# Kernel tuning notes

Hardware: AMD Instinct MI355X
Metric: run time of the kernel (lower is better)

Reference implementation:

```python
import jax, jax.numpy as jnp
import numpy as np

EMBED_DIM = 1024
N = 8192


def setup_inputs() -> dict:
    key = jax.random.key(0)
    k1, k2, k3 = jax.random.split(key, 3)
    inputs = jax.random.normal(k1, (N, EMBED_DIM), dtype=jnp.float32)
    rotation = jax.random.normal(k2, (EMBED_DIM, EMBED_DIM), dtype=jnp.float32)
    entangle = jax.random.normal(k3, (EMBED_DIM, EMBED_DIM), dtype=jnp.float32)
    return {"inputs": inputs, "rotation": rotation, "entangle": entangle}


def reference(inputs, rotation, entangle):
    # inputs: [N, D]; rotation/entangle: [D, D]
    query = inputs @ rotation          # [N, D]
    key = inputs @ entangle            # [N, D]
    scale = 1.0 / np.sqrt(inputs.shape[-1]).astype(np.float32)
    logits = (query @ key.T) * scale   # [N, N]
    scores = jax.nn.softmax(logits, axis=-1)
    return scores @ inputs             # [N, D]
```

## Files before the change

kernel.cpp:

```cpp
#include <hip/hip_runtime.h>


typedef _Float16 f16;
typedef _Float16 f16x4 __attribute__((ext_vector_type(4)));
typedef _Float16 f16x8 __attribute__((ext_vector_type(8)));
typedef float    f32x4 __attribute__((ext_vector_type(4)));
typedef unsigned int u32;

#define N_ROWS 8192
#define D_DIM  1024
#define LOG2E  1.44269504088896340736f

__device__ __forceinline__ void gload_lds16(const void* g, void* l) {
  __builtin_amdgcn_global_load_lds(
      (const __attribute__((address_space(1))) u32*)g,
      (__attribute__((address_space(3))) u32*)l, 16, 0, 0);
}

__device__ __forceinline__ f16x8 read_frag(const f16* tile, int row, int lane) {
  int kb = ((lane >> 4) & 3) << 4;
  int phys = row * 64 + (kb ^ (((row >> 1) & 3) << 4));
  return *(const f16x8*)((const char*)tile + phys);
}

__device__ __forceinline__ f16x8 read_frag64(const f16* tile, int row, int lane, int ks2) {
  int kb = ks2 * 64 + (((lane >> 4) & 3) << 4);
  int phys = row * 128 + (kb ^ ((row & 7) << 4));
  return *(const f16x8*)((const char*)tile + phys);
}

__global__ __launch_bounds__(256) void splitk(const float* __restrict__ in,
                                              f16* __restrict__ hi, f16* __restrict__ lo,
                                              int n4) {
  int i = blockIdx.x * 256 + threadIdx.x;
  if (i >= n4) return;
  float4 v = ((const float4*)in)[i];
  float vv[4] = {v.x, v.y, v.z, v.w};
  f16x4 h, l;
#pragma unroll
  for (int j = 0; j < 4; ++j) {
    f16 hh = (f16)vv[j];
    h[j] = hh;
    l[j] = (f16)(vv[j] - (float)hh);
  }
  *(f16x4*)(hi + (size_t)i * 4) = h;
  *(f16x4*)(lo + (size_t)i * 4) = l;
}

__global__ __launch_bounds__(256) void transpose_cast(const float* __restrict__ X,
                                                      f16* __restrict__ Xt) {
  __shared__ float tile[32][33];
  int bx = blockIdx.x, by = blockIdx.y;
  int tx = threadIdx.x & 31, ty0 = threadIdx.x >> 5;
#pragma unroll
  for (int r = 0; r < 4; ++r) {
    int ty = ty0 + r * 8;
    tile[ty][tx] = X[(size_t)(by * 32 + ty) * D_DIM + bx * 32 + tx];
  }
  __syncthreads();
#pragma unroll
  for (int r = 0; r < 4; ++r) {
    int ty = ty0 + r * 8;
    Xt[(size_t)(bx * 32 + ty) * N_ROWS + by * 32 + tx] = (f16)tile[tx][ty];
  }
}

__global__ __launch_bounds__(256) void gemm_abt_s(
    const f16* __restrict__ Ahi, const f16* __restrict__ Alo,
    const f16* __restrict__ Bhi, const f16* __restrict__ Blo,
    int Ncols, f16* __restrict__ Chi, f16* __restrict__ Clo) {
  __shared__ __align__(16) f16 lds[4 * 4096];
  const int t = threadIdx.x, w = t >> 6, l = t & 63;
  const int bn = blockIdx.x, bm = blockIdx.y;
  const int wr = (w >> 1) * 64, wc = (w & 1) * 64;
  const char* srcs[4];
  srcs[0] = (const char*)(Ahi + (size_t)bm * 128 * 1024);
  srcs[1] = (const char*)(Alo + (size_t)bm * 128 * 1024);
  srcs[2] = (const char*)(Bhi + (size_t)bn * 128 * 1024);
  srcs[3] = (const char*)(Blo + (size_t)bn * 128 * 1024);
  f32x4 acc[4][4] = {};
  for (int ks = 0; ks < 32; ++ks) {
#pragma unroll
    for (int tt = 0; tt < 4; ++tt)
#pragma unroll
      for (int j = 0; j < 2; ++j) {
        int seg = j * 4 + w;
        int p = seg * 1024 + l * 16;
        int r = p >> 6;
        int sw = (p & 63) ^ (((r >> 1) & 3) << 4);
        gload_lds16(srcs[tt] + (size_t)r * 2048 + ks * 64 + sw,
                    (char*)lds + tt * 8192 + seg * 1024);
      }
    __syncthreads();
    f16x8 ah[4], al[4], bh[4], bl[4];
#pragma unroll
    for (int m = 0; m < 4; ++m) {
      int row = wr + m * 16 + (l & 15);
      ah[m] = read_frag(lds, row, l);
      al[m] = read_frag(lds + 4096, row, l);
    }
#pragma unroll
    for (int n = 0; n < 4; ++n) {
      int row = wc + n * 16 + (l & 15);
      bh[n] = read_frag(lds + 8192, row, l);
      bl[n] = read_frag(lds + 12288, row, l);
    }
#pragma unroll
    for (int m = 0; m < 4; ++m)
#pragma unroll
      for (int n = 0; n < 4; ++n) {
        acc[m][n] = __builtin_amdgcn_mfma_f32_16x16x32_f16(ah[m], bh[n], acc[m][n], 0, 0, 0);
        acc[m][n] = __builtin_amdgcn_mfma_f32_16x16x32_f16(ah[m], bl[n], acc[m][n], 0, 0, 0);
        acc[m][n] = __builtin_amdgcn_mfma_f32_16x16x32_f16(al[m], bh[n], acc[m][n], 0, 0, 0);
      }
    __syncthreads();
  }
#pragma unroll
  for (int m = 0; m < 4; ++m)
#pragma unroll
    for (int n = 0; n < 4; ++n)
#pragma unroll
      for (int j = 0; j < 4; ++j) {
        int row = bm * 128 + wr + m * 16 + ((l >> 4) << 2) + j;
        int col = bn * 128 + wc + n * 16 + (l & 15);
        float v = acc[m][n][j];
        size_t idx = (size_t)row * Ncols + col;
        f16 hh = (f16)v;
        Chi[idx] = hh;
        Clo[idx] = (f16)(v - (float)hh);
      }
}

__global__ __launch_bounds__(512, 2) void gemm_abt_big(
    const f16* __restrict__ Ahi, const f16* __restrict__ Alo,
    const f16* __restrict__ Bhi, const f16* __restrict__ Blo,
    float scale, float* __restrict__ C) {
  __shared__ __align__(16) f16 lds[2][4 * 8192];
  const int t = threadIdx.x, w = t >> 6, l = t & 63;
  const int bn = blockIdx.x, bm = blockIdx.y;
  const int wm = w >> 2, wn = w & 3;
  const char* srcs[4];
  srcs[0] = (const char*)(Ahi + (size_t)bm * 256 * 1024);
  srcs[1] = (const char*)(Alo + (size_t)bm * 256 * 1024);
  srcs[2] = (const char*)(Bhi + (size_t)bn * 256 * 1024);
  srcs[3] = (const char*)(Blo + (size_t)bn * 256 * 1024);

#define STAGE_BIG(buf, kt)                                                   \
  {                                                                          \
    _Pragma("unroll") for (int rnd = 0; rnd < 8; ++rnd) {                    \
      int phys = rnd * 8192 + t * 16;           \
      int tile = phys >> 14;                                                 \
      int r = (phys & 16383) >> 6;                                           \
      int q = phys & 63;                                                     \
      int sw = q ^ (((r >> 1) & 3) << 4);                                    \
      gload_lds16(srcs[tile] + (size_t)r * 2048 + (kt) * 64 + sw,            \
                  (char*)&lds[buf][0] + phys);                               \
    }                                                                        \
  }

  f32x4 acc[8][4] = {};
  STAGE_BIG(0, 0);
  __syncthreads();
  int cur = 0;
  for (int kt = 0; kt < 32; ++kt) {
    if (kt < 31) STAGE_BIG(cur ^ 1, kt + 1);
    const f16* Lb = &lds[cur][0];
    f16x8 bh[4], bl[4];
#pragma unroll
    for (int n = 0; n < 4; ++n) {
      int row = wn * 64 + n * 16 + (l & 15);
      bh[n] = read_frag(Lb + 16384, row, l);
      bl[n] = read_frag(Lb + 24576, row, l);
    }
#pragma unroll
    for (int m = 0; m < 8; ++m) {
      int row = wm * 128 + m * 16 + (l & 15);
      f16x8 ah = read_frag(Lb, row, l);
      f16x8 al = read_frag(Lb + 8192, row, l);
#pragma unroll
      for (int n = 0; n < 4; ++n) {
        acc[m][n] = __builtin_amdgcn_mfma_f32_16x16x32_f16(ah, bh[n], acc[m][n], 0, 0, 0);
        acc[m][n] = __builtin_amdgcn_mfma_f32_16x16x32_f16(ah, bl[n], acc[m][n], 0, 0, 0);
        acc[m][n] = __builtin_amdgcn_mfma_f32_16x16x32_f16(al, bh[n], acc[m][n], 0, 0, 0);
      }
    }
    __syncthreads();
    cur ^= 1;
  }
#undef STAGE_BIG
#pragma unroll
  for (int m = 0; m < 8; ++m)
#pragma unroll
    for (int n = 0; n < 4; ++n)
#pragma unroll
      for (int j = 0; j < 4; ++j) {
        int row = bm * 256 + wm * 128 + m * 16 + ((l >> 4) << 2) + j;
        int col = bn * 256 + wn * 64 + n * 16 + (l & 15);
        C[(size_t)row * N_ROWS + col] = acc[m][n][j] * scale;
      }
}

__global__ __launch_bounds__(256) void pexp(const float* __restrict__ L,
                                            f16* __restrict__ P) {
  const int row = blockIdx.x, t = threadIdx.x, w = t >> 6, l = t & 63;
  const float4* p = (const float4*)(L + (size_t)row * N_ROWS);
  __shared__ float red[8];
  float4 v[8];
#pragma unroll
  for (int i = 0; i < 8; ++i) v[i] = p[t + i * 256];
  float mx = -3.4e38f;
#pragma unroll
  for (int i = 0; i < 8; ++i)
    mx = fmaxf(mx, fmaxf(fmaxf(v[i].x, v[i].y), fmaxf(v[i].z, v[i].w)));
#pragma unroll
  for (int off = 32; off; off >>= 1) mx = fmaxf(mx, __shfl_xor(mx, off));
  if (l == 0) red[w] = mx;
  __syncthreads();
  mx = fmaxf(fmaxf(red[0], red[1]), fmaxf(red[2], red[3]));
  float e[8][4];
  float s = 0.f;
#pragma unroll
  for (int i = 0; i < 8; ++i) {
    e[i][0] = exp2f((v[i].x - mx) * LOG2E);
    e[i][1] = exp2f((v[i].y - mx) * LOG2E);
    e[i][2] = exp2f((v[i].z - mx) * LOG2E);
    e[i][3] = exp2f((v[i].w - mx) * LOG2E);
    s += (e[i][0] + e[i][1]) + (e[i][2] + e[i][3]);
  }
#pragma unroll
  for (int off = 32; off; off >>= 1) s += __shfl_xor(s, off);
  if (l == 0) red[4 + w] = s;
  __syncthreads();
  float sinv = 1.0f / (red[4] + red[5] + red[6] + red[7]);
  f16* prow = P + (size_t)row * 16384;
#pragma unroll
  for (int i = 0; i < 8; ++i) {
    f16x4 h;
    h[0] = (f16)(e[i][0] * sinv);
    h[1] = (f16)(e[i][1] * sinv);
    h[2] = (f16)(e[i][2] * sinv);
    h[3] = (f16)(e[i][3] * sinv);
    *(f16x4*)(prow + (size_t)(t + i * 256) * 4) = h;
  }
}

__global__ __launch_bounds__(256) void gemm_pv(
    const f16* __restrict__ P,
    const f16* __restrict__ Xt,
    float* __restrict__ out) {
  __shared__ __align__(16) f16 ldsA[64 * 64];
  __shared__ __align__(16) f16 ldsB[128 * 64];
  const int t = threadIdx.x, w = t >> 6, l = t & 63;
  const int bn = blockIdx.x, bm = blockIdx.y;
  const int wr = (w >> 1) * 32, wc = (w & 1) * 64;
  const char* Abase = (const char*)(P + (size_t)bm * 64 * 16384);
  const char* Bbase = (const char*)(Xt + (size_t)bn * 128 * 8192);
  f32x4 acc[2][4] = {};
  for (int ks = 0; ks < 128; ++ks) {
#pragma unroll
    for (int s = 0; s < 2; ++s) {
      int p = s * 4096 + t * 16;
      int r = p >> 7, q = p & 127;
      int sq = q ^ ((r & 7) << 4);
      gload_lds16(Abase + (size_t)r * 32768 + ks * 128 + sq, (char*)ldsA + p);
    }
#pragma unroll
    for (int s = 0; s < 4; ++s) {
      int p = s * 4096 + t * 16;
      int r = p >> 7, q = p & 127;
      int sq = q ^ ((r & 7) << 4);
      gload_lds16(Bbase + (size_t)r * 16384 + ks * 128 + sq, (char*)ldsB + p);
    }
    __syncthreads();
#pragma unroll
    for (int ks2 = 0; ks2 < 2; ++ks2) {
      f16x8 a[2], b[4];
#pragma unroll
      for (int m = 0; m < 2; ++m) a[m] = read_frag64(ldsA, wr + m * 16 + (l & 15), l, ks2);
#pragma unroll
      for (int n = 0; n < 4; ++n) b[n] = read_frag64(ldsB, wc + n * 16 + (l & 15), l, ks2);
#pragma unroll
      for (int m = 0; m < 2; ++m)
#pragma unroll
        for (int n = 0; n < 4; ++n)
          acc[m][n] = __builtin_amdgcn_mfma_f32_16x16x32_f16(a[m], b[n], acc[m][n], 0, 0, 0);
    }
    __syncthreads();
  }
#pragma unroll
  for (int m = 0; m < 2; ++m)
#pragma unroll
    for (int n = 0; n < 4; ++n)
#pragma unroll
      for (int j = 0; j < 4; ++j) {
        int row = bm * 64 + wr + m * 16 + ((l >> 4) << 2) + j;
        int col = bn * 128 + wc + n * 16 + (l & 15);
        out[(size_t)row * D_DIM + col] = acc[m][n][j];
      }
}

extern "C" void kernel_launch(void* const* d_in, const int* in_sizes, int n_in,
                              void* d_out, int out_size, void* d_ws, size_t ws_size,
                              hipStream_t stream) {
  const float* X = (const float*)d_in[0];
  const float* R = (const float*)d_in[1];
  const float* E = (const float*)d_in[2];
  float* out = (float*)d_out;

  char* p = (char*)d_ws;
  auto alloc = [&](size_t bytes) -> char* {
    char* r = p;
    p += (bytes + 255) & ~(size_t)255;
    return r;
  };
  f16* Xhi = (f16*)alloc((size_t)N_ROWS * D_DIM * 2);
  f16* Xlo = (f16*)alloc((size_t)N_ROWS * D_DIM * 2);
  f16* Yhi = (f16*)alloc((size_t)N_ROWS * D_DIM * 2);
  f16* Ylo = (f16*)alloc((size_t)N_ROWS * D_DIM * 2);
  f16* Xt  = (f16*)alloc((size_t)N_ROWS * D_DIM * 2);
  float* Lbuf = (float*)p;
  size_t front = (size_t)(p - (char*)d_ws);

  char* tail = (char*)d_ws + ws_size;
  auto alloct = [&](size_t bytes) -> char* {
    tail = (char*)(((uintptr_t)tail - bytes) & ~(uintptr_t)255);
    return tail;
  };
  f16* Rhi  = (f16*)alloct((size_t)D_DIM * D_DIM * 2);
  f16* Rlo  = (f16*)alloct((size_t)D_DIM * D_DIM * 2);
  f16* Ehi  = (f16*)alloct((size_t)D_DIM * D_DIM * 2);
  f16* Elo  = (f16*)alloct((size_t)D_DIM * D_DIM * 2);
  f16* Mthi = (f16*)alloct((size_t)D_DIM * D_DIM * 2);
  f16* Mtlo = (f16*)alloct((size_t)D_DIM * D_DIM * 2);

  size_t avail = ws_size > front ? ws_size - front : 0;
  int CH = (int)(avail / ((size_t)N_ROWS * 4));
  if (CH > N_ROWS) CH = N_ROWS;
  CH &= ~255;
  if (CH < 256) CH = 256;

  splitk<<<dim3((N_ROWS * D_DIM / 4 + 255) / 256), 256, 0, stream>>>(X, Xhi, Xlo, N_ROWS * D_DIM / 4);
  splitk<<<dim3((D_DIM * D_DIM / 4 + 255) / 256), 256, 0, stream>>>(R, Rhi, Rlo, D_DIM * D_DIM / 4);
  splitk<<<dim3((D_DIM * D_DIM / 4 + 255) / 256), 256, 0, stream>>>(E, Ehi, Elo, D_DIM * D_DIM / 4);
  transpose_cast<<<dim3(D_DIM / 32, N_ROWS / 32), 256, 0, stream>>>(X, Xt);

  gemm_abt_s<<<dim3(8, 8), 256, 0, stream>>>(Ehi, Elo, Rhi, Rlo, D_DIM, Mthi, Mtlo);
  gemm_abt_s<<<dim3(8, 64), 256, 0, stream>>>(Xhi, Xlo, Mthi, Mtlo, D_DIM, Yhi, Ylo);

  for (int c0 = 0; c0 < N_ROWS; c0 += CH) {
    int rows = (N_ROWS - c0 < CH) ? (N_ROWS - c0) : CH;
    gemm_abt_big<<<dim3(N_ROWS / 256, rows / 256), 512, 0, stream>>>(
        Yhi + (size_t)c0 * D_DIM, Ylo + (size_t)c0 * D_DIM, Xhi, Xlo,
        0.03125f, Lbuf);
    pexp<<<dim3(rows), 256, 0, stream>>>(Lbuf, (f16*)Lbuf);
    gemm_pv<<<dim3(D_DIM / 128, rows / 64), 256, 0, stream>>>(
        (const f16*)Lbuf, Xt, out + (size_t)c0 * D_DIM);
  }
}
```

Before: 776.7 us.

## Interleave next-tile staging with MFMA phases in the split-fp16 logits GEMM

The main k-loop of the big A·B^T GEMM is split into four phases. Each phase issues a quarter of the next tile's global-to-LDS loads, reads its own A fragments, and runs its MFMAs at raised wave priority, separated by explicit barriers and sched_barriers. The aim is to spread memory traffic across the compute phases and keep loads overlapped with MFMA work instead of issuing one large burst per iteration. The cost is extra barriers per k-step, and the manual waitcnt handling makes correctness of the LDS double buffer depend on careful ordering.

```diff
diff --git a/kernel.cpp b/kernel.cpp
--- a/kernel.cpp
+++ b/kernel.cpp
@@ -145,49 +145,71 @@
   srcs[2] = (const char*)(Bhi + (size_t)bn * 256 * 1024);
   srcs[3] = (const char*)(Blo + (size_t)bn * 256 * 1024);
 
-#define STAGE_BIG(buf, kt)                                                   \
+#define STAGE_Q(buf, kt, q)                                                  \
   {                                                                          \
-    _Pragma("unroll") for (int rnd = 0; rnd < 8; ++rnd) {                    \
-      int phys = rnd * 8192 + t * 16;           \
-      int tile = phys >> 14;                                                 \
+    _Pragma("unroll") for (int rr = 0; rr < 2; ++rr) {                       \
+      int phys = ((q)*2 + rr) * 8192 + t * 16;                               \
       int r = (phys & 16383) >> 6;                                           \
-      int q = phys & 63;                                                     \
-      int sw = q ^ (((r >> 1) & 3) << 4);                                    \
-      gload_lds16(srcs[tile] + (size_t)r * 2048 + (kt) * 64 + sw,            \
+      int sw = (phys & 63) ^ (((r >> 1) & 3) << 4);                          \
+      gload_lds16(srcs[q] + (size_t)r * 2048 + (kt)*64 + sw,                 \
                   (char*)&lds[buf][0] + phys);                               \
     }                                                                        \
   }
 
   f32x4 acc[8][4] = {};
-  STAGE_BIG(0, 0);
+  STAGE_Q(0, 0, 0); STAGE_Q(0, 0, 1); STAGE_Q(0, 0, 2); STAGE_Q(0, 0, 3);
   __syncthreads();
   int cur = 0;
   for (int kt = 0; kt < 32; ++kt) {
-    if (kt < 31) STAGE_BIG(cur ^ 1, kt + 1);
     const f16* Lb = &lds[cur][0];
+    const int nxt = cur ^ 1;
     f16x8 bh[4], bl[4];
 #pragma unroll
-    for (int n = 0; n < 4; ++n) {
-      int row = wn * 64 + n * 16 + (l & 15);
-      bh[n] = read_frag(Lb + 16384, row, l);
-      bl[n] = read_frag(Lb + 24576, row, l);
-    }
-#pragma unroll
-    for (int m = 0; m < 8; ++m) {
-      int row = wm * 128 + m * 16 + (l & 15);
-      f16x8 ah = read_frag(Lb, row, l);
-      f16x8 al = read_frag(Lb + 8192, row, l);
-#pragma unroll
-      for (int n = 0; n < 4; ++n) {
-        acc[m][n] = __builtin_amdgcn_mfma_f32_16x16x32_f16(ah, bh[n], acc[m][n], 0, 0, 0);
-        acc[m][n] = __builtin_amdgcn_mfma_f32_16x16x32_f16(ah, bl[n], acc[m][n], 0, 0, 0);
-        acc[m][n] = __builtin_amdgcn_mfma_f32_16x16x32_f16(al, bh[n], acc[m][n], 0, 0, 0);
-      }
-    }
-    __syncthreads();
+    for (int ph = 0; ph < 4; ++ph) {
+      f16x8 a0h, a0l, a1h, a1l;
+      {
+        int row0 = wm * 128 + (ph * 2) * 16 + (l & 15);
+        a0h = read_frag(Lb, row0, l);
+        a0l = read_frag(Lb + 8192, row0, l);
+        a1h = read_frag(Lb, row0 + 16, l);
+        a1l = read_frag(Lb + 8192, row0 + 16, l);
+      }
+      if (ph == 0) {
+#pragma unroll
+        for (int n = 0; n < 4; ++n) {
+          int rowb = wn * 64 + n * 16 + (l & 15);
+          bh[n] = read_frag(Lb + 16384, rowb, l);
+          bl[n] = read_frag(Lb + 24576, rowb, l);
+        }
+      }
+      if (kt < 31) STAGE_Q(nxt, kt + 1, ph);
+      __builtin_amdgcn_s_barrier();
+      asm volatile("s_waitcnt lgkmcnt(0)" ::: "memory");
+      __builtin_amdgcn_sched_barrier(0);
+      __builtin_amdgcn_s_setprio(1);
+#pragma unroll
+      for (int mm = 0; mm < 2; ++mm) {
+        const f16x8 ah = mm ? a1h : a0h;
+        const f16x8 al = mm ? a1l : a0l;
+        const int m = ph * 2 + mm;
+#pragma unroll
+        for (int n = 0; n < 4; ++n) {
+          acc[m][n] = __builtin_amdgcn_mfma_f32_16x16x32_f16(ah, bh[n], acc[m][n], 0, 0, 0);
+          acc[m][n] = __builtin_amdgcn_mfma_f32_16x16x32_f16(ah, bl[n], acc[m][n], 0, 0, 0);
+          acc[m][n] = __builtin_amdgcn_mfma_f32_16x16x32_f16(al, bh[n], acc[m][n], 0, 0, 0);
+        }
+      }
+      __builtin_amdgcn_s_setprio(0);
+      __builtin_amdgcn_sched_barrier(0);
+      if (ph == 3) {
+        asm volatile("s_waitcnt vmcnt(0)" ::: "memory");
+      }
+      __builtin_amdgcn_s_barrier();
+      __builtin_amdgcn_sched_barrier(0);
+    }
     cur ^= 1;
   }
-#undef STAGE_BIG
+#undef STAGE_Q
 #pragma unroll
   for (int m = 0; m < 8; ++m)
 #pragma unroll
```

New measurement: 807.4 us. 1.04x slower.

## Double-buffer and enlarge PV GEMM tiles; reuse big GEMM for Y projection

Applied to the files above, without the earlier changes.

The P·X GEMM now uses 128x128 block tiles with 4x4 MFMA accumulators per wave and double-buffered LDS staging, so the next K slice loads while the current one computes. The X·M^T projection that produced Y moves from the small 128-tile kernel to the 256-tile double-buffered big GEMM, which is templated to write split hi/lo fp16 output. The aim is more data reuse per block and less load latency exposed in both GEMMs. The costs are more registers and LDS per block and fewer blocks: 32 for the Y projection, and half as many for PV, which may leave CUs idle.

```diff
diff --git a/kernel.cpp b/kernel.cpp
--- a/kernel.cpp
+++ b/kernel.cpp
@@ -131,10 +131,12 @@
       }
 }
 
+template <int OUT_SPLIT>
 __global__ __launch_bounds__(512, 2) void gemm_abt_big(
     const f16* __restrict__ Ahi, const f16* __restrict__ Alo,
     const f16* __restrict__ Bhi, const f16* __restrict__ Blo,
-    float scale, float* __restrict__ C) {
+    float scale, int Ncols,
+    float* __restrict__ C, f16* __restrict__ Chi, f16* __restrict__ Clo) {
   __shared__ __align__(16) f16 lds[2][4 * 8192];
   const int t = threadIdx.x, w = t >> 6, l = t & 63;
   const int bn = blockIdx.x, bm = blockIdx.y;
@@ -153,7 +155,7 @@
       int r = (phys & 16383) >> 6;                                           \
       int q = phys & 63;                                                     \
       int sw = q ^ (((r >> 1) & 3) << 4);                                    \
-      gload_lds16(srcs[tile] + (size_t)r * 2048 + (kt) * 64 + sw,            \
+      gload_lds16(srcs[tile] + (size_t)r * 2048 + (kt)*64 + sw,              \
                   (char*)&lds[buf][0] + phys);                               \
     }                                                                        \
   }
@@ -196,7 +198,15 @@
       for (int j = 0; j < 4; ++j) {
         int row = bm * 256 + wm * 128 + m * 16 + ((l >> 4) << 2) + j;
         int col = bn * 256 + wn * 64 + n * 16 + (l & 15);
-        C[(size_t)row * N_ROWS + col] = acc[m][n][j] * scale;
+        float v = acc[m][n][j] * scale;
+        size_t idx = (size_t)row * Ncols + col;
+        if (OUT_SPLIT) {
+          f16 hh = (f16)v;
+          Chi[idx] = hh;
+          Clo[idx] = (f16)(v - (float)hh);
+        } else {
+          C[idx] = v;
+        }
       }
 }
 
@@ -248,52 +258,57 @@
     const f16* __restrict__ P,
     const f16* __restrict__ Xt,
     float* __restrict__ out) {
-  __shared__ __align__(16) f16 ldsA[64 * 64];
-  __shared__ __align__(16) f16 ldsB[128 * 64];
+  __shared__ __align__(16) f16 lds[2][16384];
   const int t = threadIdx.x, w = t >> 6, l = t & 63;
   const int bn = blockIdx.x, bm = blockIdx.y;
-  const int wr = (w >> 1) * 32, wc = (w & 1) * 64;
-  const char* Abase = (const char*)(P + (size_t)bm * 64 * 16384);
+  const int wr = (w >> 1) * 64, wc = (w & 1) * 64;
+  const char* Abase = (const char*)(P + (size_t)bm * 128 * 16384);
   const char* Bbase = (const char*)(Xt + (size_t)bn * 128 * 8192);
-  f32x4 acc[2][4] = {};
+
+#define STAGE_PV(buf, ks)                                                    \
+  {                                                                          \
+    _Pragma("unroll") for (int i = 0; i < 4; ++i) {                          \
+      int phys = i * 4096 + t * 16;                                          \
+      int r = phys >> 7, q = phys & 127;                                     \
+      int sq = q ^ ((r & 7) << 4);                                           \
+      gload_lds16(Abase + (size_t)r * 32768 + (ks)*128 + sq,                 \
+                  (char*)&lds[buf][0] + phys);                               \
+      gload_lds16(Bbase + (size_t)r * 16384 + (ks)*128 + sq,                 \
+                  (char*)&lds[buf][8192] + phys);                            \
+    }                                                                        \
+  }
+
+  f32x4 acc[4][4] = {};
+  STAGE_PV(0, 0);
+  __syncthreads();
+  int cur = 0;
   for (int ks = 0; ks < 128; ++ks) {
-#pragma unroll
-    for (int s = 0; s < 2; ++s) {
-      int p = s * 4096 + t * 16;
-      int r = p >> 7, q = p & 127;
-      int sq = q ^ ((r & 7) << 4);
-      gload_lds16(Abase + (size_t)r * 32768 + ks * 128 + sq, (char*)ldsA + p);
-    }
-#pragma unroll
-    for (int s = 0; s < 4; ++s) {
-      int p = s * 4096 + t * 16;
-      int r = p >> 7, q = p & 127;
-      int sq = q ^ ((r & 7) << 4);
-      gload_lds16(Bbase + (size_t)r * 16384 + ks * 128 + sq, (char*)ldsB + p);
-    }
-    __syncthreads();
+    if (ks < 127) STAGE_PV(cur ^ 1, ks + 1);
+    const f16* Lb = &lds[cur][0];
 #pragma unroll
     for (int ks2 = 0; ks2 < 2; ++ks2) {
-      f16x8 a[2], b[4];
-#pragma unroll
-      for (int m = 0; m < 2; ++m) a[m] = read_frag64(ldsA, wr + m * 16 + (l & 15), l, ks2);
-#pragma unroll
-      for (int n = 0; n < 4; ++n) b[n] = read_frag64(ldsB, wc + n * 16 + (l & 15), l, ks2);
-#pragma unroll
-      for (int m = 0; m < 2; ++m)
+      f16x8 a[4], b[4];
+#pragma unroll
+      for (int m = 0; m < 4; ++m) a[m] = read_frag64(Lb, wr + m * 16 + (l & 15), l, ks2);
+#pragma unroll
+      for (int n = 0; n < 4; ++n) b[n] = read_frag64(Lb + 8192, wc + n * 16 + (l & 15), l, ks2);
+#pragma unroll
+      for (int m = 0; m < 4; ++m)
 #pragma unroll
         for (int n = 0; n < 4; ++n)
           acc[m][n] = __builtin_amdgcn_mfma_f32_16x16x32_f16(a[m], b[n], acc[m][n], 0, 0, 0);
     }
     __syncthreads();
-  }
-#pragma unroll
-  for (int m = 0; m < 2; ++m)
+    cur ^= 1;
+  }
+#undef STAGE_PV
+#pragma unroll
+  for (int m = 0; m < 4; ++m)
 #pragma unroll
     for (int n = 0; n < 4; ++n)
 #pragma unroll
       for (int j = 0; j < 4; ++j) {
-        int row = bm * 64 + wr + m * 16 + ((l >> 4) << 2) + j;
+        int row = bm * 128 + wr + m * 16 + ((l >> 4) << 2) + j;
         int col = bn * 128 + wc + n * 16 + (l & 15);
         out[(size_t)row * D_DIM + col] = acc[m][n][j];
       }
@@ -345,15 +360,16 @@
   transpose_cast<<<dim3(D_DIM / 32, N_ROWS / 32), 256, 0, stream>>>(X, Xt);
 
   gemm_abt_s<<<dim3(8, 8), 256, 0, stream>>>(Ehi, Elo, Rhi, Rlo, D_DIM, Mthi, Mtlo);
-  gemm_abt_s<<<dim3(8, 64), 256, 0, stream>>>(Xhi, Xlo, Mthi, Mtlo, D_DIM, Yhi, Ylo);
+  gemm_abt_big<1><<<dim3(D_DIM / 256, N_ROWS / 256), 512, 0, stream>>>(
+      Xhi, Xlo, Mthi, Mtlo, 1.0f, D_DIM, nullptr, Yhi, Ylo);
 
   for (int c0 = 0; c0 < N_ROWS; c0 += CH) {
     int rows = (N_ROWS - c0 < CH) ? (N_ROWS - c0) : CH;
-    gemm_abt_big<<<dim3(N_ROWS / 256, rows / 256), 512, 0, stream>>>(
+    gemm_abt_big<0><<<dim3(N_ROWS / 256, rows / 256), 512, 0, stream>>>(
         Yhi + (size_t)c0 * D_DIM, Ylo + (size_t)c0 * D_DIM, Xhi, Xlo,
-        0.03125f, Lbuf);
+        0.03125f, N_ROWS, Lbuf, nullptr, nullptr);
     pexp<<<dim3(rows), 256, 0, stream>>>(Lbuf, (f16*)Lbuf);
-    gemm_pv<<<dim3(D_DIM / 128, rows / 64), 256, 0, stream>>>(
+    gemm_pv<<<dim3(D_DIM / 128, rows / 128), 256, 0, stream>>>(
         (const f16*)Lbuf, Xt, out + (size_t)c0 * D_DIM);
   }
 }
```

New measurement: 802.6 us. 1.03x slower.

## Interleave prefetch with MFMA phases in QK GEMM and double-buffer PV GEMM

Applied to the files above, without the earlier changes.

The big QK^T GEMM's k-step is split into four sub-phases. Each phase loads a subset of fragments, issues half of the next tile's global-to-LDS loads during the first two phases, and runs its MFMAs at raised wave priority, using explicit barriers and waitcnts. The PV GEMM goes from single-buffered LDS with a sync every step to a double-buffered prefetch of the next K slice, so loads overlap compute. This adds barriers per k-step and doubles PV's LDS footprint, which could lower occupancy.

```diff
diff --git a/kernel.cpp b/kernel.cpp
--- a/kernel.cpp
+++ b/kernel.cpp
@@ -145,49 +145,67 @@
   srcs[2] = (const char*)(Bhi + (size_t)bn * 256 * 1024);
   srcs[3] = (const char*)(Blo + (size_t)bn * 256 * 1024);
 
-#define STAGE_BIG(buf, kt)                                                   \
+#define STAGE_HALF(buf, kt, h)                                               \
   {                                                                          \
-    _Pragma("unroll") for (int rnd = 0; rnd < 8; ++rnd) {                    \
-      int phys = rnd * 8192 + t * 16;           \
+    _Pragma("unroll") for (int rnd = (h) * 4; rnd < (h) * 4 + 4; ++rnd) {    \
+      int phys = rnd * 8192 + t * 16;                                        \
       int tile = phys >> 14;                                                 \
       int r = (phys & 16383) >> 6;                                           \
       int q = phys & 63;                                                     \
       int sw = q ^ (((r >> 1) & 3) << 4);                                    \
-      gload_lds16(srcs[tile] + (size_t)r * 2048 + (kt) * 64 + sw,            \
+      gload_lds16(srcs[tile] + (size_t)r * 2048 + (kt)*64 + sw,              \
                   (char*)&lds[buf][0] + phys);                               \
     }                                                                        \
   }
 
   f32x4 acc[8][4] = {};
-  STAGE_BIG(0, 0);
+  STAGE_HALF(0, 0, 0);
+  STAGE_HALF(0, 0, 1);
   __syncthreads();
   int cur = 0;
   for (int kt = 0; kt < 32; ++kt) {
-    if (kt < 31) STAGE_BIG(cur ^ 1, kt + 1);
     const f16* Lb = &lds[cur][0];
-    f16x8 bh[4], bl[4];
-#pragma unroll
-    for (int n = 0; n < 4; ++n) {
-      int row = wn * 64 + n * 16 + (l & 15);
-      bh[n] = read_frag(Lb + 16384, row, l);
-      bl[n] = read_frag(Lb + 24576, row, l);
+    const int nxt = cur ^ 1;
+#pragma unroll
+    for (int ph = 0; ph < 4; ++ph) {
+      const int mh = ph >> 1, nh = ph & 1;
+      f16x8 ah[4], al[4], bh2[2], bl2[2];
+#pragma unroll
+      for (int i = 0; i < 4; ++i) {
+        int row = wm * 128 + (mh * 4 + i) * 16 + (l & 15);
+        ah[i] = read_frag(Lb, row, l);
+        al[i] = read_frag(Lb + 8192, row, l);
+      }
+#pragma unroll
+      for (int j = 0; j < 2; ++j) {
+        int row = wn * 64 + (nh * 2 + j) * 16 + (l & 15);
+        bh2[j] = read_frag(Lb + 16384, row, l);
+        bl2[j] = read_frag(Lb + 24576, row, l);
+      }
+      if (kt < 31 && ph < 2) STAGE_HALF(nxt, kt + 1, ph);
+      __builtin_amdgcn_s_barrier();
+      asm volatile("s_waitcnt lgkmcnt(0)" ::: "memory");
+      __builtin_amdgcn_sched_barrier(0);
+      __builtin_amdgcn_s_setprio(1);
+#pragma unroll
+      for (int i = 0; i < 4; ++i)
+#pragma unroll
+        for (int j = 0; j < 2; ++j) {
+          const int m = mh * 4 + i, n = nh * 2 + j;
+          acc[m][n] = __builtin_amdgcn_mfma_f32_16x16x32_f16(ah[i], bh2[j], acc[m][n], 0, 0, 0);
+          acc[m][n] = __builtin_amdgcn_mfma_f32_16x16x32_f16(ah[i], bl2[j], acc[m][n], 0, 0, 0);
+          acc[m][n] = __builtin_amdgcn_mfma_f32_16x16x32_f16(al[i], bh2[j], acc[m][n], 0, 0, 0);
+        }
+      __builtin_amdgcn_s_setprio(0);
+      __builtin_amdgcn_sched_barrier(0);
+      if (ph == 3) {
+        asm volatile("s_waitcnt vmcnt(0)" ::: "memory");
+      }
+      __builtin_amdgcn_s_barrier();
     }
-#pragma unroll
-    for (int m = 0; m < 8; ++m) {
-      int row = wm * 128 + m * 16 + (l & 15);
-      f16x8 ah = read_frag(Lb, row, l);
-      f16x8 al = read_frag(Lb + 8192, row, l);
-#pragma unroll
-      for (int n = 0; n < 4; ++n) {
-        acc[m][n] = __builtin_amdgcn_mfma_f32_16x16x32_f16(ah, bh[n], acc[m][n], 0, 0, 0);
-        acc[m][n] = __builtin_amdgcn_mfma_f32_16x16x32_f16(ah, bl[n], acc[m][n], 0, 0, 0);
-        acc[m][n] = __builtin_amdgcn_mfma_f32_16x16x32_f16(al, bh[n], acc[m][n], 0, 0, 0);
-      }
-    }
-    __syncthreads();
     cur ^= 1;
   }
-#undef STAGE_BIG
+#undef STAGE_HALF
 #pragma unroll
   for (int m = 0; m < 8; ++m)
 #pragma unroll
@@ -248,37 +266,45 @@
     const f16* __restrict__ P,
     const f16* __restrict__ Xt,
     float* __restrict__ out) {
-  __shared__ __align__(16) f16 ldsA[64 * 64];
-  __shared__ __align__(16) f16 ldsB[128 * 64];
+  __shared__ __align__(16) f16 lds[2][12288];
   const int t = threadIdx.x, w = t >> 6, l = t & 63;
   const int bn = blockIdx.x, bm = blockIdx.y;
   const int wr = (w >> 1) * 32, wc = (w & 1) * 64;
   const char* Abase = (const char*)(P + (size_t)bm * 64 * 16384);
   const char* Bbase = (const char*)(Xt + (size_t)bn * 128 * 8192);
+
+#define STAGE_PV(buf, ks)                                                    \
+  {                                                                          \
+    _Pragma("unroll") for (int i = 0; i < 2; ++i) {                          \
+      int phys = i * 4096 + t * 16;                                          \
+      int r = phys >> 7, q = phys & 127;                                     \
+      int sq = q ^ ((r & 7) << 4);                                           \
+      gload_lds16(Abase + (size_t)r * 32768 + (ks)*128 + sq,                 \
+                  (char*)&lds[buf][0] + phys);                               \
+    }                                                                        \
+    _Pragma("unroll") for (int i = 0; i < 4; ++i) {                          \
+      int phys = i * 4096 + t * 16;                                          \
+      int r = phys >> 7, q = phys & 127;                                     \
+      int sq = q ^ ((r & 7) << 4);                                           \
+      gload_lds16(Bbase + (size_t)r * 16384 + (ks)*128 + sq,                 \
+                  (char*)&lds[buf][4096] + phys);                            \
+    }                                                                        \
+  }
+
   f32x4 acc[2][4] = {};
+  STAGE_PV(0, 0);
+  __syncthreads();
+  int cur = 0;
   for (int ks = 0; ks < 128; ++ks) {
-#pragma unroll
-    for (int s = 0; s < 2; ++s) {
-      int p = s * 4096 + t * 16;
-      int r = p >> 7, q = p & 127;
-      int sq = q ^ ((r & 7) << 4);
-      gload_lds16(Abase + (size_t)r * 32768 + ks * 128 + sq, (char*)ldsA + p);
-    }
-#pragma unroll
-    for (int s = 0; s < 4; ++s) {
-      int p = s * 4096 + t * 16;
-      int r = p >> 7, q = p & 127;
-      int sq = q ^ ((r & 7) << 4);
-      gload_lds16(Bbase + (size_t)r * 16384 + ks * 128 + sq, (char*)ldsB + p);
-    }
-    __syncthreads();
+    if (ks < 127) STAGE_PV(cur ^ 1, ks + 1);
+    const f16* Lb = &lds[cur][0];
 #pragma unroll
     for (int ks2 = 0; ks2 < 2; ++ks2) {
       f16x8 a[2], b[4];
 #pragma unroll
-      for (int m = 0; m < 2; ++m) a[m] = read_frag64(ldsA, wr + m * 16 + (l & 15), l, ks2);
-#pragma unroll
-      for (int n = 0; n < 4; ++n) b[n] = read_frag64(ldsB, wc + n * 16 + (l & 15), l, ks2);
+      for (int m = 0; m < 2; ++m) a[m] = read_frag64(Lb, wr + m * 16 + (l & 15), l, ks2);
+#pragma unroll
+      for (int n = 0; n < 4; ++n) b[n] = read_frag64(Lb + 4096, wc + n * 16 + (l & 15), l, ks2);
 #pragma unroll
       for (int m = 0; m < 2; ++m)
 #pragma unroll
@@ -286,7 +312,9 @@
           acc[m][n] = __builtin_amdgcn_mfma_f32_16x16x32_f16(a[m], b[n], acc[m][n], 0, 0, 0);
     }
     __syncthreads();
-  }
+    cur ^= 1;
+  }
+#undef STAGE_PV
 #pragma unroll
   for (int m = 0; m < 2; ++m)
 #pragma unroll
```

New measurement: 838.4 us. 1.08x slower.
